# Kernel tuning notes

Hardware: AMD Instinct MI355X
Metric: run time of the kernel (lower is better)

The kernel has to match this reference:

```python
import jax, jax.numpy as jnp
import numpy as np

KSIZE = 13
BETA = 0.97
THR = 1.0
SMIN, SMAX = 0.4, 10.0


def gaussian_kernel(sigma):
    # matches torch: coarse grid [-6,6] (13 pts), normalized by sum over fine grid [-60,60] (130 pts)
    r = jnp.linspace(-(KSIZE // 2), KSIZE // 2, KSIZE)
    r_all = jnp.linspace(-(KSIZE // 2) * 10.0, (KSIZE // 2) * 10.0, KSIZE * 10)
    k = jnp.exp(-0.5 * (r / sigma) ** 2)
    norm = jnp.sum(jnp.exp(-0.5 * (r_all / sigma) ** 2))
    return k / norm


def setup_inputs() -> dict:
    key = jax.random.key(0)
    k1, = jax.random.split(key, 1)
    B, C, T = 512, 224, 224
    inp = jax.random.normal(k1, (B, 1, C, T), dtype=jnp.float32)
    w = jnp.float32((SMIN + SMAX) / 2.0)  # 5.2, init value of nn.Parameter
    return {"inp": inp, "w": w}


def reference(inp, w):
    x = inp[:, 0]                      # (B, C, T)
    B, C, T = x.shape
    wc = jnp.clip(w, SMIN, SMAX)
    kern = gaussian_kernel(wc)          # (K,), symmetric
    pad = (KSIZE - 1) // 2

    # gaussian smoothing across the channel axis, same kernel for every t and b
    # x_mean[b,c,t] = sum_k kern[k] * pad_C(x)[b, c+k, t]
    xc = x.transpose(0, 2, 1).reshape(B * T, 1, C)   # (B*T, 1, C)
    xm = jax.lax.conv_general_dilated(
        xc, kern.reshape(1, 1, KSIZE),
        window_strides=(1,), padding=[(pad, pad)],
        dimension_numbers=("NCH", "OIH", "NCH"))
    x_mean = xm.reshape(B, T, C).transpose(0, 2, 1)  # (B, C, T)

    # input current: clip x at the smoothed mean from above
    I = x - jax.nn.relu(x - x_mean)                   # (B, C, T)

    # snn.Leaky (beta=0.97, threshold=1, reset_mechanism='subtract')
    def step(mem, I_t):
        reset = (mem > THR).astype(mem.dtype)         # reset based on previous mem
        mem = BETA * mem + I_t - reset * THR
        spk = (mem > THR).astype(mem.dtype)           # Heaviside(mem - threshold)
        return mem, spk

    mem0 = jnp.zeros((B, C), x.dtype)
    _, spk = jax.lax.scan(step, mem0, I.transpose(2, 0, 1))  # (T, B, C)
    spk = spk.transpose(1, 2, 0)[:, None]                    # (B, 1, C, T)
    return spk
```

## Files before the change

kernel.cpp:

```cpp
#include <hip/hip_runtime.h>

constexpr int Cc = 224;
constexpr int Tt = 224;
constexpr int TT = 32;
constexpr int NTILE = Tt / TT;
constexpr int SROWS = 128;
constexpr int SLABWORDS = SROWS * TT;
constexpr int BDIM = 128;

#define GLDS16(src, dst) __builtin_amdgcn_global_load_lds( \
    (const __attribute__((address_space(1))) unsigned int*)(src), \
    (__attribute__((address_space(3))) unsigned int*)(dst), 16, 0, 0)

__global__ __launch_bounds__(BDIM)
void cgss_snn_kernel(const float* __restrict__ x,
                     const float* __restrict__ wp,
                     float* __restrict__ out)
{
    __shared__ float lds[2 * 2 * SLABWORDS];

    const int tid = threadIdx.x;
    const int w   = tid >> 6;
    const int l   = tid & 63;
    const int b   = blockIdx.x;

    float* slab = &lds[w * 2 * SLABWORDS];
    const long long bofs = (long long)b * Cc * Tt;
    const float* xb = x + bofs;
    float*       ob = out + bofs;

    const int cbase = 112 * w - 8;

    {
        const int zj = (w == 0) ? 0 : 15;
        float4 z = make_float4(0.f, 0.f, 0.f, 0.f);
        *reinterpret_cast<float4*>(&slab[0 * SLABWORDS + zj * 256 + l * 4]) = z;
        *reinterpret_cast<float4*>(&slab[1 * SLABWORDS + zj * 256 + l * 4]) = z;
    }

    const int jbeg = (w == 0) ? 1 : 0;
    const int jend = (w == 0) ? 16 : 15;
    const int srow = l >> 3;
    const int sc   = l & 7;

    auto stage = [&](int buf, int t0) {
        for (int j = jbeg; j < jend; ++j) {
            int r  = 8 * j + srow;
            int tq = sc ^ ((r >> 1) & 7);
            const float* src = xb + (cbase + r) * Tt + t0 + tq * 4;
            float* dst = &slab[buf * SLABWORDS + j * 256];
            GLDS16(src, dst);
        }
    };

    stage(0, 0);

    float kr[13];
    {
        float wv = wp[0];
        float wc = fminf(fmaxf(wv, 0.4f), 10.0f);
        float norm = 0.0f;
        const float step = 120.0f / 129.0f;
        for (int j = 0; j < 130; ++j) {
            float r = -60.0f + (float)j * step;
            float z = r / wc;
            norm += expf(-0.5f * z * z);
        }
        for (int i = 0; i < 13; ++i) {
            float r = (float)(i - 6);
            float z = r / wc;
            kr[i] = expf(-0.5f * z * z) / norm;
        }
    }

    float mem0 = 0.f, mem1 = 0.f, rst0 = 0.f, rst1 = 0.f;
    const int c0 = 112 * w + 2 * l;
    int buf = 0;

    asm volatile("s_waitcnt vmcnt(0)" ::: "memory");
    __builtin_amdgcn_sched_barrier(0);

    for (int tile = 0; tile < NTILE; ++tile) {
        const int t0 = tile * TT;
        if (tile < NTILE - 1) stage(buf ^ 1, t0 + TT);

        if (l < 56) {
            const float* sb = &slab[buf * SLABWORDS];
            const int rb = 2 * l + 2;
#pragma unroll 2
            for (int tq = 0; tq < 8; ++tq) {
                float4 val[14];
#pragma unroll
                for (int k = 0; k < 14; ++k) {
                    int r = rb + k;
                    int q = tq ^ ((r >> 1) & 7);
                    val[k] = *reinterpret_cast<const float4*>(&sb[r * 32 + q * 4]);
                }
                float4 a0 = make_float4(0,0,0,0), a1 = make_float4(0,0,0,0);
#pragma unroll
                for (int i = 0; i < 13; ++i) {
                    float kk = kr[i];
                    a0.x += kk * val[i].x;    a0.y += kk * val[i].y;
                    a0.z += kk * val[i].z;    a0.w += kk * val[i].w;
                    a1.x += kk * val[i+1].x;  a1.y += kk * val[i+1].y;
                    a1.z += kk * val[i+1].z;  a1.w += kk * val[i+1].w;
                }
                float4 s0, s1;
                {
                    const float* xv = (const float*)&val[6];
                    const float* av = (const float*)&a0;
                    float*       sv = (float*)&s0;
#pragma unroll
                    for (int s = 0; s < 4; ++s) {
                        float d  = xv[s] - av[s];
                        float rl = d > 0.0f ? d : 0.0f;
                        float I  = xv[s] - rl;
                        mem0 = 0.97f * mem0 + I - rst0;
                        float spk = (mem0 > 1.0f) ? 1.0f : 0.0f;
                        rst0 = spk;
                        sv[s] = spk;
                    }
                }
                {
                    const float* xv = (const float*)&val[7];
                    const float* av = (const float*)&a1;
                    float*       sv = (float*)&s1;
#pragma unroll
                    for (int s = 0; s < 4; ++s) {
                        float d  = xv[s] - av[s];
                        float rl = d > 0.0f ? d : 0.0f;
                        float I  = xv[s] - rl;
                        mem1 = 0.97f * mem1 + I - rst1;
                        float spk = (mem1 > 1.0f) ? 1.0f : 0.0f;
                        rst1 = spk;
                        sv[s] = spk;
                    }
                }
                const int t = t0 + tq * 4;
                *reinterpret_cast<float4*>(&ob[(long long)c0 * Tt + t])       = s0;
                *reinterpret_cast<float4*>(&ob[(long long)(c0 + 1) * Tt + t]) = s1;
            }
        }

        asm volatile("s_waitcnt vmcnt(0)" ::: "memory");
        __builtin_amdgcn_sched_barrier(0);
        buf ^= 1;
    }
}

extern "C" void kernel_launch(void* const* d_in, const int* in_sizes, int n_in,
                              void* d_out, int out_size, void* d_ws, size_t ws_size,
                              hipStream_t stream)
{
    const float* x  = (const float*)d_in[0];
    const float* w  = (const float*)d_in[1];
    float* out      = (float*)d_out;
    const int B = in_sizes[0] / (Cc * Tt);
    cgss_snn_kernel<<<B, BDIM, 0, stream>>>(x, w, out);
}
```

Before: 67.26 us.

## Restructure to one channel per thread with LDS-staged coalesced spike stores

Moves from 128 threads with two channels per lane to 256 threads with one channel per thread. The whole 236-row padded slab is shared across the block instead of per-wave slabs with halo duplication. Spikes are packed into a bitmask, written back into the consumed LDS buffer, then read out so each wave stores full contiguous 128-byte row segments to global memory. This targets the strided per-thread float4 output stores and the redundant halo loads, at the cost of extra block-wide barriers per tile and an LDS round trip.

```diff
diff --git a/kernel.cpp b/kernel.cpp
--- a/kernel.cpp
+++ b/kernel.cpp
@@ -1,55 +1,53 @@
 #include <hip/hip_runtime.h>
 
-constexpr int Cc = 224;
-constexpr int Tt = 224;
-constexpr int TT = 32;
-constexpr int NTILE = Tt / TT;
-constexpr int SROWS = 128;
-constexpr int SLABWORDS = SROWS * TT;
-constexpr int BDIM = 128;
+constexpr int Cc   = 224;
+constexpr int Tt   = 224;
+constexpr int TT   = 32;
+constexpr int NT   = Tt / TT;
+constexpr int ROWS = 236;
+constexpr int BUFW = ROWS * TT;
+constexpr int BDIM = 256;
 
 #define GLDS16(src, dst) __builtin_amdgcn_global_load_lds( \
     (const __attribute__((address_space(1))) unsigned int*)(src), \
     (__attribute__((address_space(3))) unsigned int*)(dst), 16, 0, 0)
 
-__global__ __launch_bounds__(BDIM)
+
+__global__ __launch_bounds__(BDIM, 2)
 void cgss_snn_kernel(const float* __restrict__ x,
                      const float* __restrict__ wp,
                      float* __restrict__ out)
 {
-    __shared__ float lds[2 * 2 * SLABWORDS];
+    __shared__ float lds[2 * BUFW];
 
     const int tid = threadIdx.x;
     const int w   = tid >> 6;
     const int l   = tid & 63;
     const int b   = blockIdx.x;
-
-    float* slab = &lds[w * 2 * SLABWORDS];
-    const long long bofs = (long long)b * Cc * Tt;
+    const long long bofs = (long long)b * (Cc * Tt);
     const float* xb = x + bofs;
     float*       ob = out + bofs;
 
-    const int cbase = 112 * w - 8;
-
-    {
-        const int zj = (w == 0) ? 0 : 15;
+    if (tid < 192) {
+        int bufi = tid / 96;
+        int q    = tid - 96 * bufi;
+        int rr   = q >> 3;
+        int slot = q & 7;
+        int row  = (rr < 6) ? rr : (224 + rr);
         float4 z = make_float4(0.f, 0.f, 0.f, 0.f);
-        *reinterpret_cast<float4*>(&slab[0 * SLABWORDS + zj * 256 + l * 4]) = z;
-        *reinterpret_cast<float4*>(&slab[1 * SLABWORDS + zj * 256 + l * 4]) = z;
+        *reinterpret_cast<float4*>(&lds[bufi * BUFW + row * 32 + slot * 4]) = z;
     }
 
-    const int jbeg = (w == 0) ? 1 : 0;
-    const int jend = (w == 0) ? 16 : 15;
     const int srow = l >> 3;
-    const int sc   = l & 7;
-
-    auto stage = [&](int buf, int t0) {
-        for (int j = jbeg; j < jend; ++j) {
-            int r  = 8 * j + srow;
-            int tq = sc ^ ((r >> 1) & 7);
-            const float* src = xb + (cbase + r) * Tt + t0 + tq * 4;
-            float* dst = &slab[buf * SLABWORDS + j * 256];
-            GLDS16(src, dst);
+    const int stq  = (l & 7) ^ ((6 + srow) & 7);
+    auto stage = [&](int bufi, int t0) {
+        float* base = &lds[bufi * BUFW];
+#pragma unroll
+        for (int i = 0; i < 7; ++i) {
+            int j   = 7 * w + i;
+            int row = 6 + 8 * j + srow;
+            const float* src = xb + (row - 6) * Tt + t0 + stq * 4;
+            GLDS16(src, &base[(6 + 8 * j) * 32]);
         }
     };
 
@@ -73,78 +71,81 @@
         }
     }
 
-    float mem0 = 0.f, mem1 = 0.f, rst0 = 0.f, rst1 = 0.f;
-    const int c0 = 112 * w + 2 * l;
-    int buf = 0;
+    float mem = 0.0f, rstv = 0.0f;
+    int bufc = 0;
 
     asm volatile("s_waitcnt vmcnt(0)" ::: "memory");
-    __builtin_amdgcn_sched_barrier(0);
+    __syncthreads();
 
-    for (int tile = 0; tile < NTILE; ++tile) {
+    for (int tile = 0; tile < NT; ++tile) {
         const int t0 = tile * TT;
-        if (tile < NTILE - 1) stage(buf ^ 1, t0 + TT);
+        if (tile < NT - 1) stage(bufc ^ 1, t0 + TT);
 
-        if (l < 56) {
-            const float* sb = &slab[buf * SLABWORDS];
-            const int rb = 2 * l + 2;
+        unsigned m = 0;
+        if (tid < Cc) {
+            const char* sb = (const char*)&lds[bufc * BUFW];
 #pragma unroll 2
             for (int tq = 0; tq < 8; ++tq) {
-                float4 val[14];
+                float4 v[13];
 #pragma unroll
-                for (int k = 0; k < 14; ++k) {
-                    int r = rb + k;
-                    int q = tq ^ ((r >> 1) & 7);
-                    val[k] = *reinterpret_cast<const float4*>(&sb[r * 32 + q * 4]);
+                for (int k = 0; k < 13; ++k) {
+                    int row = tid + k;
+                    v[k] = *reinterpret_cast<const float4*>(
+                        sb + row * 128 + ((tq ^ (row & 7)) << 4));
                 }
-                float4 a0 = make_float4(0,0,0,0), a1 = make_float4(0,0,0,0);
+                float4 acc = make_float4(0.f, 0.f, 0.f, 0.f);
 #pragma unroll
-                for (int i = 0; i < 13; ++i) {
-                    float kk = kr[i];
-                    a0.x += kk * val[i].x;    a0.y += kk * val[i].y;
-                    a0.z += kk * val[i].z;    a0.w += kk * val[i].w;
-                    a1.x += kk * val[i+1].x;  a1.y += kk * val[i+1].y;
-                    a1.z += kk * val[i+1].z;  a1.w += kk * val[i+1].w;
+                for (int k = 0; k < 13; ++k) {
+                    float kk = kr[k];
+                    acc.x += kk * v[k].x;  acc.y += kk * v[k].y;
+                    acc.z += kk * v[k].z;  acc.w += kk * v[k].w;
                 }
-                float4 s0, s1;
-                {
-                    const float* xv = (const float*)&val[6];
-                    const float* av = (const float*)&a0;
-                    float*       sv = (float*)&s0;
+                const float* xv = (const float*)&v[6];
+                const float* av = (const float*)&acc;
 #pragma unroll
-                    for (int s = 0; s < 4; ++s) {
-                        float d  = xv[s] - av[s];
-                        float rl = d > 0.0f ? d : 0.0f;
-                        float I  = xv[s] - rl;
-                        mem0 = 0.97f * mem0 + I - rst0;
-                        float spk = (mem0 > 1.0f) ? 1.0f : 0.0f;
-                        rst0 = spk;
-                        sv[s] = spk;
-                    }
+                for (int s = 0; s < 4; ++s) {
+                    float d  = xv[s] - av[s];
+                    float rl = d > 0.0f ? d : 0.0f;
+                    float I  = xv[s] - rl;
+                    mem = 0.97f * mem + I - rstv;
+                    bool sp = mem > 1.0f;
+                    rstv = sp ? 1.0f : 0.0f;
+                    m |= sp ? (1u << (4 * tq + s)) : 0u;
                 }
-                {
-                    const float* xv = (const float*)&val[7];
-                    const float* av = (const float*)&a1;
-                    float*       sv = (float*)&s1;
+            }
+        }
+        __syncthreads();
+
+        if (tid < Cc) {
+            char* sb = (char*)&lds[bufc * BUFW];
 #pragma unroll
-                    for (int s = 0; s < 4; ++s) {
-                        float d  = xv[s] - av[s];
-                        float rl = d > 0.0f ? d : 0.0f;
-                        float I  = xv[s] - rl;
-                        mem1 = 0.97f * mem1 + I - rst1;
-                        float spk = (mem1 > 1.0f) ? 1.0f : 0.0f;
-                        rst1 = spk;
-                        sv[s] = spk;
-                    }
-                }
-                const int t = t0 + tq * 4;
-                *reinterpret_cast<float4*>(&ob[(long long)c0 * Tt + t])       = s0;
-                *reinterpret_cast<float4*>(&ob[(long long)(c0 + 1) * Tt + t]) = s1;
+            for (int tq = 0; tq < 8; ++tq) {
+                float4 sv;
+                sv.x = (m >> (4 * tq + 0)) & 1 ? 1.0f : 0.0f;
+                sv.y = (m >> (4 * tq + 1)) & 1 ? 1.0f : 0.0f;
+                sv.z = (m >> (4 * tq + 2)) & 1 ? 1.0f : 0.0f;
+                sv.w = (m >> (4 * tq + 3)) & 1 ? 1.0f : 0.0f;
+                *reinterpret_cast<float4*>(
+                    sb + tid * 128 + ((tq ^ (tid & 7)) << 4)) = sv;
+            }
+        }
+        __syncthreads();
+
+        {
+            const char* sb = (const char*)&lds[bufc * BUFW];
+            const int s = l & 7;
+#pragma unroll
+            for (int i = 0; i < 7; ++i) {
+                int cr = 8 * (7 * w + i) + (l >> 3);
+                float4 v = *reinterpret_cast<const float4*>(
+                    sb + cr * 128 + ((s ^ (cr & 7)) << 4));
+                *reinterpret_cast<float4*>(&ob[(long long)cr * Tt + t0 + 4 * s]) = v;
             }
         }
 
         asm volatile("s_waitcnt vmcnt(0)" ::: "memory");
-        __builtin_amdgcn_sched_barrier(0);
-        buf ^= 1;
+        __syncthreads();
+        bufc ^= 1;
     }
 }
 
```

After: 75.36 us. 12.0% more time.
